# Kernel tuning notes

Measured on AMD Instinct MI355X. Metric: run time of the kernel, lower is better.

Reference implementation:

```python
import jax, jax.numpy as jnp
import numpy as np

KEEP_RATIO = 0.7  # fully-annealed keep ratio (epoch >= 2*warmup_epochs)


def setup_inputs() -> dict:
    key = jax.random.key(0)
    k0, k1, k2 = jax.random.split(key, 3)
    B, H, W, C, HID = 16, 128, 128, 256, 128
    N = H * W
    tokens = jax.random.normal(k0, (B, N, C), dtype=jnp.float32)
    # xavier_uniform-ish init for the scorer MLP
    lim1 = float(np.sqrt(6.0 / (C + HID)))
    lim2 = float(np.sqrt(6.0 / (HID + 1)))
    w1 = jax.random.uniform(k1, (C, HID), minval=-lim1, maxval=lim1, dtype=jnp.float32)
    b1 = jnp.zeros((HID,), dtype=jnp.float32)
    w2 = jax.random.uniform(k2, (HID, 1), minval=-lim2, maxval=lim2, dtype=jnp.float32)
    b2 = jnp.zeros((1,), dtype=jnp.float32)
    return {"tokens": tokens, "w1": w1, "b1": b1, "w2": w2, "b2": b2}


def reference(tokens, w1, b1, w2, b2):
    # tokens: [B, N, C]; importance scorer: fc1 -> GELU(exact) -> fc2 -> squeeze
    B, N, C = tokens.shape
    num_keep = int(N * KEEP_RATIO)  # static; min_tokens=10 << num_keep
    h = jax.nn.gelu(jnp.einsum("bnc,ch->bnh", tokens, w1) + b1, approximate=False)
    scores = (jnp.einsum("bnh,ho->bno", h, w2) + b2)[..., 0]  # [B, N]
    # top-k token selection, then sort kept indices to preserve spatial order
    _, top_idx = jax.lax.top_k(scores, num_keep)          # [B, K]
    kept_indices = jnp.sort(top_idx, axis=-1)              # [B, K]
    pruned_tokens = jnp.take_along_axis(tokens, kept_indices[..., None], axis=1)  # [B, K, C]
    return pruned_tokens, kept_indices, scores
```

## Files before the change

kernel.cpp:

```cpp
#include <hip/hip_runtime.h>
#include <math.h>

#define B_ 16
#define N_ 16384
#define C_ 256
#define H_ 128
#define K_ 11468
#define G_ ((B_ * N_) / 16)
#define GPB_ 16
#define NBLK_ (G_ / GPB_)

typedef __attribute__((ext_vector_type(8))) short s16x8;
typedef __attribute__((ext_vector_type(4))) float f32x4;
typedef __attribute__((ext_vector_type(4))) unsigned int u32x4;

__device__ __forceinline__ unsigned short f2bf(float f) {
  unsigned u = __builtin_bit_cast(unsigned, f);
  return (unsigned short)((u + 0x7FFFu + ((u >> 16) & 1u)) >> 16);
}
__device__ __forceinline__ unsigned fkey(float f) {
  unsigned u = __builtin_bit_cast(unsigned, f);
  return (u & 0x80000000u) ? ~u : (u | 0x80000000u);
}
__device__ __forceinline__ unsigned pk2(float hi, float lo) {
  return __builtin_amdgcn_perm(__builtin_bit_cast(unsigned, hi),
                               __builtin_bit_cast(unsigned, lo), 0x07060302u);
}

#define LDS_BARRIER()                                     \
  do {                                                    \
    asm volatile("s_waitcnt lgkmcnt(0)" ::: "memory");    \
    __builtin_amdgcn_s_barrier();                         \
  } while (0)

__device__ __forceinline__ float gelu_fast(float h) {
  const float t = 0.5f * h * h;
  const float u = 0.147f * t;
  const float num = t * (1.2732395f + u);
  const float den = 1.0f + u;
  const float r = num * __builtin_amdgcn_rcpf(den);
  const float e = __builtin_amdgcn_exp2f(r * -1.44269504f);
  const float s = __builtin_amdgcn_sqrtf(fmaxf(1.0f - e, 0.0f));
  const unsigned sgn = __builtin_bit_cast(unsigned, h) & 0x80000000u;
  const float erfv = __builtin_bit_cast(float, __builtin_bit_cast(unsigned, s) | sgn);
  return 0.5f * h * (1.0f + erfv);
}

__global__ void k_prep(const float* __restrict__ w1, unsigned short* __restrict__ w1t) {
  int i = blockIdx.x * blockDim.x + threadIdx.x;
  if (i < C_ * H_) {
    int c = i / H_, h = i % H_;
    w1t[h * C_ + c] = f2bf(w1[i]);
  }
}

__global__ __launch_bounds__(256) void k_score(
    const float* __restrict__ tokens, const unsigned short* __restrict__ w1t,
    const float* __restrict__ b1, const float* __restrict__ w2,
    const float* __restrict__ b2, float* __restrict__ scores_out) {
  __shared__ unsigned short lds_a[2][8 * 64 * 8];
  __shared__ float lds_c[4][16];

  const int tid = threadIdx.x;
  const int lane = tid & 63;
  const int l15 = lane & 15;
  const int l4 = lane >> 4;
  const int w = tid >> 6;

  s16x8 bfr0[8], bfr1[8];
  const int row0 = (2 * w) * 16 + l15;
  const int row1 = row0 + 16;
#pragma unroll
  for (int kk = 0; kk < 8; ++kk) {
    bfr0[kk] = *reinterpret_cast<const s16x8*>(w1t + row0 * 256 + (l4 + 4 * kk) * 8);
    bfr1[kk] = *reinterpret_cast<const s16x8*>(w1t + row1 * 256 + (l4 + 4 * kk) * 8);
  }
  const float b1v0 = b1[row0], b1v1 = b1[row1];
  const float w2v0 = w2[row0], w2v1 = w2[row1];
  const float b2v = b2[0];

  const int t = tid & 15;
  const int s = tid >> 4;
  const int g0 = blockIdx.x * GPB_;
  const float* tg = tokens + ((size_t)(g0 * 16 + t)) * 256 + s * 16;
  const int lb0 = (2 * s) * 128 + t * 8;
  const int lb1 = lb0 + 128;

  f32x4 vv[4];
  {
#pragma unroll
    for (int q = 0; q < 4; ++q) vv[q] = *reinterpret_cast<const f32x4*>(tg + 4 * q);
    u32x4 o0, o1;
    o0[0] = pk2(vv[0][1], vv[0][0]);
    o0[1] = pk2(vv[0][3], vv[0][2]);
    o0[2] = pk2(vv[1][1], vv[1][0]);
    o0[3] = pk2(vv[1][3], vv[1][2]);
    o1[0] = pk2(vv[2][1], vv[2][0]);
    o1[1] = pk2(vv[2][3], vv[2][2]);
    o1[2] = pk2(vv[3][1], vv[3][0]);
    o1[3] = pk2(vv[3][3], vv[3][2]);
    *reinterpret_cast<u32x4*>(&lds_a[0][lb0]) = o0;
    *reinterpret_cast<u32x4*>(&lds_a[0][lb1]) = o1;
  }
  LDS_BARRIER();

  int cur = 0;
  for (int i = 0; i < GPB_; ++i) {
    const int g = g0 + i;
    if (i + 1 < GPB_) {
      const float* p = tg + (size_t)(i + 1) * 4096;
#pragma unroll
      for (int q = 0; q < 4; ++q) vv[q] = *reinterpret_cast<const f32x4*>(p + 4 * q);
    }

    f32x4 acc0 = (f32x4){0.f, 0.f, 0.f, 0.f};
    f32x4 acc1 = (f32x4){0.f, 0.f, 0.f, 0.f};
#pragma unroll
    for (int kk = 0; kk < 8; ++kk) {
      s16x8 a = *reinterpret_cast<const s16x8*>(&lds_a[cur][(kk * 64 + lane) * 8]);
      acc0 = __builtin_amdgcn_mfma_f32_16x16x32_bf16(a, bfr0[kk], acc0, 0, 0, 0);
      acc1 = __builtin_amdgcn_mfma_f32_16x16x32_bf16(a, bfr1[kk], acc1, 0, 0, 0);
    }

    float p4[4];
#pragma unroll
    for (int rr = 0; rr < 4; ++rr) {
      float sp = gelu_fast(acc0[rr] + b1v0) * w2v0 + gelu_fast(acc1[rr] + b1v1) * w2v1;
      sp += __shfl_xor(sp, 1);
      sp += __shfl_xor(sp, 2);
      sp += __shfl_xor(sp, 4);
      sp += __shfl_xor(sp, 8);
      p4[rr] = sp;
    }
    if (l15 == 0) {
#pragma unroll
      for (int rr = 0; rr < 4; ++rr) lds_c[w][l4 * 4 + rr] = p4[rr];
    }
    LDS_BARRIER();

    if (tid < 16) {
      scores_out[g * 16 + tid] =
          lds_c[0][tid] + lds_c[1][tid] + lds_c[2][tid] + lds_c[3][tid] + b2v;
    }
    if (i + 1 < GPB_) {
      u32x4 o0, o1;
      o0[0] = pk2(vv[0][1], vv[0][0]);
      o0[1] = pk2(vv[0][3], vv[0][2]);
      o0[2] = pk2(vv[1][1], vv[1][0]);
      o0[3] = pk2(vv[1][3], vv[1][2]);
      o1[0] = pk2(vv[2][1], vv[2][0]);
      o1[1] = pk2(vv[2][3], vv[2][2]);
      o1[2] = pk2(vv[3][1], vv[3][0]);
      o1[3] = pk2(vv[3][3], vv[3][2]);
      *reinterpret_cast<u32x4*>(&lds_a[cur ^ 1][lb0]) = o0;
      *reinterpret_cast<u32x4*>(&lds_a[cur ^ 1][lb1]) = o1;
    }
    LDS_BARRIER();
    cur ^= 1;
  }
}

__device__ unsigned block_exscan_1024(unsigned v, volatile unsigned* wsum) {
  const int tid = threadIdx.x;
  const int lane = tid & 63;
  const int w = tid >> 6;
  unsigned x = v;
#pragma unroll
  for (int d = 1; d < 64; d <<= 1) {
    unsigned t = __shfl_up(x, d);
    if (lane >= d) x += t;
  }
  if (lane == 63) wsum[w] = x;
  __syncthreads();
  if (tid < 16) {
    unsigned s = wsum[tid];
#pragma unroll
    for (int d = 1; d < 16; d <<= 1) {
      unsigned u = __shfl_up(s, d);
      if (tid >= d) s += u;
    }
    wsum[tid] = s;
  }
  __syncthreads();
  unsigned r = (w ? wsum[w - 1] : 0u) + x - v;
  __syncthreads();
  return r;
}

__global__ __launch_bounds__(1024) void k_select(const float* __restrict__ scores_f,
                                                 int* __restrict__ kept,
                                                 float* __restrict__ out_idx) {
  __shared__ unsigned hist[2048];
  __shared__ unsigned wsum[16];
  __shared__ unsigned sh_T, sh_need;
  const int b = blockIdx.x;
  const int tid = threadIdx.x;
  const float* sp = scores_f + (size_t)b * N_;

  hist[tid] = 0; hist[tid + 1024] = 0;
  __syncthreads();
  for (int i = tid; i < N_; i += 1024) atomicAdd(&hist[fkey(sp[i]) >> 21], 1u);
  __syncthreads();
  {
    const int hi = 2047 - 2 * tid, lo = hi - 1;
    const unsigned chi = hist[hi], pair = chi + hist[lo];
    unsigned before = block_exscan_1024(pair, wsum);
    if (before < K_ && before + chi >= K_) { sh_T = (unsigned)hi; sh_need = K_ - before; }
    else if (before + chi < K_ && before + pair >= K_) { sh_T = (unsigned)lo; sh_need = K_ - before - chi; }
  }
  __syncthreads();
  const unsigned T0 = sh_T;
  unsigned needK = sh_need;
  __syncthreads();

  hist[tid] = 0; hist[tid + 1024] = 0;
  __syncthreads();
  for (int i = tid; i < N_; i += 1024) {
    unsigned k = fkey(sp[i]);
    if ((k >> 21) == T0) atomicAdd(&hist[(k >> 10) & 2047u], 1u);
  }
  __syncthreads();
  {
    const int hi = 2047 - 2 * tid, lo = hi - 1;
    const unsigned chi = hist[hi], pair = chi + hist[lo];
    unsigned before = block_exscan_1024(pair, wsum);
    if (before < needK && before + chi >= needK) { sh_T = (unsigned)hi; sh_need = needK - before; }
    else if (before + chi < needK && before + pair >= needK) { sh_T = (unsigned)lo; sh_need = needK - before - chi; }
  }
  __syncthreads();
  const unsigned P21 = (T0 << 11) | sh_T;
  needK = sh_need;
  __syncthreads();

  hist[tid] = 0;
  __syncthreads();
  for (int i = tid; i < N_; i += 1024) {
    unsigned k = fkey(sp[i]);
    if ((k >> 10) == P21) atomicAdd(&hist[k & 1023u], 1u);
  }
  __syncthreads();
  {
    const int hi = 1023 - tid;
    const unsigned chi = hist[hi];
    unsigned before = block_exscan_1024(chi, wsum);
    if (before < needK && before + chi >= needK) { sh_T = (unsigned)hi; sh_need = needK - before; }
  }
  __syncthreads();
  const unsigned Tkey = (P21 << 10) | sh_T;
  const unsigned need = sh_need;
  __syncthreads();

  const int i0 = tid * 16;
  unsigned cgt = 0, ceq = 0;
  for (int j = 0; j < 16; ++j) {
    unsigned k = fkey(sp[i0 + j]);
    cgt += (k > Tkey);
    ceq += (k == Tkey);
  }
  unsigned packed = block_exscan_1024((cgt << 16) | ceq, wsum);
  unsigned gt_b = packed >> 16;
  unsigned eq_b = packed & 0xFFFFu;
  for (int j = 0; j < 16; ++j) {
    unsigned k = fkey(sp[i0 + j]);
    if (k > Tkey) {
      unsigned pos = gt_b + (eq_b < need ? eq_b : need);
      kept[(size_t)b * K_ + pos] = i0 + j;
      out_idx[(size_t)b * K_ + pos] = (float)(i0 + j);
      ++gt_b;
    } else if (k == Tkey) {
      if (eq_b < need) {
        unsigned pos = gt_b + eq_b;
        kept[(size_t)b * K_ + pos] = i0 + j;
        out_idx[(size_t)b * K_ + pos] = (float)(i0 + j);
      }
      ++eq_b;
    }
  }
}

__global__ __launch_bounds__(256) void k_gather(const float* __restrict__ tokens,
                                                const int* __restrict__ kept,
                                                float* __restrict__ outp) {
  const int wid = (blockIdx.x * blockDim.x + threadIdx.x) >> 6;
  const int lane = threadIdx.x & 63;
  if (wid >= B_ * K_) return;
  const int b = wid / K_;
  const int idx = kept[wid];
  const f32x4 v = *reinterpret_cast<const f32x4*>(tokens + ((size_t)b * N_ + idx) * C_ + lane * 4);
  *reinterpret_cast<f32x4*>(outp + (size_t)wid * C_ + lane * 4) = v;
}

extern "C" void kernel_launch(void* const* d_in, const int* in_sizes, int n_in,
                              void* d_out, int out_size, void* d_ws, size_t ws_size,
                              hipStream_t stream) {
  const float* tokens = (const float*)d_in[0];
  const float* w1 = (const float*)d_in[1];
  const float* b1 = (const float*)d_in[2];
  const float* w2 = (const float*)d_in[3];
  const float* b2 = (const float*)d_in[4];

  float* out = (float*)d_out;
  float* out_pruned = out;
  float* out_idx = out + (size_t)B_ * K_ * C_;
  float* out_scores = out_idx + (size_t)B_ * K_;

  char* ws = (char*)d_ws;
  unsigned short* w1t = (unsigned short*)ws;
  int* kept = (int*)(ws + 0x10000);

  k_prep<<<dim3((C_ * H_ + 255) / 256), dim3(256), 0, stream>>>(w1, w1t);
  k_score<<<dim3(NBLK_), dim3(256), 0, stream>>>(tokens, w1t, b1, w2, b2, out_scores);
  k_select<<<dim3(B_), dim3(1024), 0, stream>>>(out_scores, kept, out_idx);
  k_gather<<<dim3((B_ * K_ + 3) / 4), dim3(256), 0, stream>>>(tokens, kept, out_pruned);
}
```

Measured before the change: 159.2 us.

## Replace three-pass radix select with one histogram pass plus candidate ranking

```diff
diff --git a/kernel.cpp b/kernel.cpp
--- a/kernel.cpp
+++ b/kernel.cpp
@@ -192,7 +192,7 @@
                                                  float* __restrict__ out_idx) {
   __shared__ unsigned hist[2048];
   __shared__ unsigned wsum[16];
-  __shared__ unsigned sh_T, sh_need;
+  __shared__ unsigned sh_T, sh_need, sh_m;
   const int b = blockIdx.x;
   const int tid = threadIdx.x;
   const float* sp = scores_f + (size_t)b * N_;
@@ -207,73 +207,70 @@
     unsigned before = block_exscan_1024(pair, wsum);
     if (before < K_ && before + chi >= K_) { sh_T = (unsigned)hi; sh_need = K_ - before; }
     else if (before + chi < K_ && before + pair >= K_) { sh_T = (unsigned)lo; sh_need = K_ - before - chi; }
+    if (tid == 0) sh_m = 0;
   }
   __syncthreads();
   const unsigned T0 = sh_T;
-  unsigned needK = sh_need;
-  __syncthreads();
-
-  hist[tid] = 0; hist[tid + 1024] = 0;
-  __syncthreads();
-  for (int i = tid; i < N_; i += 1024) {
-    unsigned k = fkey(sp[i]);
-    if ((k >> 21) == T0) atomicAdd(&hist[(k >> 10) & 2047u], 1u);
-  }
-  __syncthreads();
-  {
-    const int hi = 2047 - 2 * tid, lo = hi - 1;
-    const unsigned chi = hist[hi], pair = chi + hist[lo];
-    unsigned before = block_exscan_1024(pair, wsum);
-    if (before < needK && before + chi >= needK) { sh_T = (unsigned)hi; sh_need = needK - before; }
-    else if (before + chi < needK && before + pair >= needK) { sh_T = (unsigned)lo; sh_need = needK - before - chi; }
-  }
-  __syncthreads();
-  const unsigned P21 = (T0 << 11) | sh_T;
-  needK = sh_need;
-  __syncthreads();
-
-  hist[tid] = 0;
-  __syncthreads();
-  for (int i = tid; i < N_; i += 1024) {
-    unsigned k = fkey(sp[i]);
-    if ((k >> 10) == P21) atomicAdd(&hist[k & 1023u], 1u);
-  }
-  __syncthreads();
-  {
-    const int hi = 1023 - tid;
-    const unsigned chi = hist[hi];
-    unsigned before = block_exscan_1024(chi, wsum);
-    if (before < needK && before + chi >= needK) { sh_T = (unsigned)hi; sh_need = needK - before; }
-  }
-  __syncthreads();
-  const unsigned Tkey = (P21 << 10) | sh_T;
   const unsigned need = sh_need;
   __syncthreads();
 
+  unsigned* cand = hist;
   const int i0 = tid * 16;
-  unsigned cgt = 0, ceq = 0;
+  unsigned cgt = 0;
   for (int j = 0; j < 16; ++j) {
     unsigned k = fkey(sp[i0 + j]);
-    cgt += (k > Tkey);
-    ceq += (k == Tkey);
-  }
-  unsigned packed = block_exscan_1024((cgt << 16) | ceq, wsum);
-  unsigned gt_b = packed >> 16;
-  unsigned eq_b = packed & 0xFFFFu;
+    unsigned bin = k >> 21;
+    cgt += (bin > T0);
+    if (bin == T0) {
+      unsigned e = atomicAdd(&sh_m, 1u);
+      if (e < 1024u) { cand[2 * e] = k; cand[2 * e + 1] = (unsigned)(i0 + j); }
+    }
+  }
+  unsigned gt_base = block_exscan_1024(cgt, wsum);
+  const unsigned m = (sh_m < 1024u) ? sh_m : 1024u;
+
+  for (unsigned e = tid; e < m; e += 1024) {
+    const unsigned ke = cand[2 * e];
+    const unsigned ie = cand[2 * e + 1] & 0x7FFFFFFFu;
+    unsigned r = 0;
+    for (unsigned f = 0; f < m; ++f) {
+      const unsigned kf = cand[2 * f];
+      const unsigned fi = cand[2 * f + 1] & 0x7FFFFFFFu;
+      r += (kf > ke) || (kf == ke && fi < ie);
+    }
+    if (r < need) cand[2 * e + 1] |= 0x80000000u;
+  }
+  __syncthreads();
+
+  unsigned gt_run = gt_base;
   for (int j = 0; j < 16; ++j) {
-    unsigned k = fkey(sp[i0 + j]);
-    if (k > Tkey) {
-      unsigned pos = gt_b + (eq_b < need ? eq_b : need);
-      kept[(size_t)b * K_ + pos] = i0 + j;
-      out_idx[(size_t)b * K_ + pos] = (float)(i0 + j);
-      ++gt_b;
-    } else if (k == Tkey) {
-      if (eq_b < need) {
-        unsigned pos = gt_b + eq_b;
-        kept[(size_t)b * K_ + pos] = i0 + j;
-        out_idx[(size_t)b * K_ + pos] = (float)(i0 + j);
+    const unsigned i = (unsigned)(i0 + j);
+    const unsigned k = fkey(sp[i0 + j]);
+    const unsigned bin = k >> 21;
+    if (bin > T0) {
+      unsigned eqb = 0;
+      for (unsigned f = 0; f < m; ++f) {
+        const unsigned fi = cand[2 * f + 1];
+        eqb += (fi >> 31) & ((fi & 0x7FFFFFFFu) < i);
       }
-      ++eq_b;
+      const unsigned pos = gt_run + eqb;
+      kept[(size_t)b * K_ + pos] = (int)i;
+      out_idx[(size_t)b * K_ + pos] = (float)i;
+      ++gt_run;
+    } else if (bin == T0) {
+      unsigned eqb = 0, sel = 0;
+      for (unsigned f = 0; f < m; ++f) {
+        const unsigned fi = cand[2 * f + 1];
+        const unsigned fidx = fi & 0x7FFFFFFFu;
+        const unsigned flg = fi >> 31;
+        eqb += flg & (fidx < i);
+        sel |= flg & (fidx == i);
+      }
+      if (sel) {
+        const unsigned pos = gt_run + eqb;
+        kept[(size_t)b * K_ + pos] = (int)i;
+        out_idx[(size_t)b * K_ + pos] = (float)i;
+      }
     }
   }
 }
```

New measurement: 238.7 us. 1.5x slower.

## Stream token tiles into LDS with async global_load_lds and convert at MFMA time

Applied to the files above, without the earlier changes.

```diff
diff --git a/kernel.cpp b/kernel.cpp
--- a/kernel.cpp
+++ b/kernel.cpp
@@ -32,6 +32,12 @@
     asm volatile("s_waitcnt lgkmcnt(0)" ::: "memory");    \
     __builtin_amdgcn_s_barrier();                         \
   } while (0)
+
+__device__ __forceinline__ void async_copy16(const float* g, float* l) {
+  __builtin_amdgcn_global_load_lds(
+      (const __attribute__((address_space(1))) unsigned int*)g,
+      (__attribute__((address_space(3))) unsigned int*)l, 16, 0, 0);
+}
 
 __device__ __forceinline__ float gelu_fast(float h) {
   const float t = 0.5f * h * h;
@@ -58,7 +64,7 @@
     const float* __restrict__ tokens, const unsigned short* __restrict__ w1t,
     const float* __restrict__ b1, const float* __restrict__ w2,
     const float* __restrict__ b2, float* __restrict__ scores_out) {
-  __shared__ unsigned short lds_a[2][8 * 64 * 8];
+  __shared__ float lds_f[2][4096];
   __shared__ float lds_c[4][16];
 
   const int tid = threadIdx.x;
@@ -79,45 +85,51 @@
   const float w2v0 = w2[row0], w2v1 = w2[row1];
   const float b2v = b2[0];
 
-  const int t = tid & 15;
-  const int s = tid >> 4;
   const int g0 = blockIdx.x * GPB_;
-  const float* tg = tokens + ((size_t)(g0 * 16 + t)) * 256 + s * 16;
-  const int lb0 = (2 * s) * 128 + t * 8;
-  const int lb1 = lb0 + 128;
-
-  f32x4 vv[4];
-  {
-#pragma unroll
-    for (int q = 0; q < 4; ++q) vv[q] = *reinterpret_cast<const f32x4*>(tg + 4 * q);
-    u32x4 o0, o1;
-    o0[0] = pk2(vv[0][1], vv[0][0]);
-    o0[1] = pk2(vv[0][3], vv[0][2]);
-    o0[2] = pk2(vv[1][1], vv[1][0]);
-    o0[3] = pk2(vv[1][3], vv[1][2]);
-    o1[0] = pk2(vv[2][1], vv[2][0]);
-    o1[1] = pk2(vv[2][3], vv[2][2]);
-    o1[2] = pk2(vv[3][1], vv[3][0]);
-    o1[3] = pk2(vv[3][3], vv[3][2]);
-    *reinterpret_cast<u32x4*>(&lds_a[0][lb0]) = o0;
-    *reinterpret_cast<u32x4*>(&lds_a[0][lb1]) = o1;
-  }
-  LDS_BARRIER();
+  const float* gbase = tokens + (size_t)g0 * 16 * 256;
+
+  int st_[4], sc_[4];
+#pragma unroll
+  for (int r = 0; r < 4; ++r) {
+    const int sslot = (w * 4 + r) * 64 + lane;
+    st_[r] = sslot & 15;
+    sc_[r] = sslot >> 4;
+  }
+
+  const int sbase = 32 * l4 + l15;
+
+#pragma unroll
+  for (int r = 0; r < 4; ++r) {
+    async_copy16(gbase + st_[r] * 256 + sc_[r] * 4,
+                 &lds_f[0][(size_t)((w * 4 + r) * 64 + lane) * 4]);
+  }
+  __syncthreads();
 
   int cur = 0;
   for (int i = 0; i < GPB_; ++i) {
     const int g = g0 + i;
     if (i + 1 < GPB_) {
-      const float* p = tg + (size_t)(i + 1) * 4096;
-#pragma unroll
-      for (int q = 0; q < 4; ++q) vv[q] = *reinterpret_cast<const f32x4*>(p + 4 * q);
-    }
-
+      const float* gp = gbase + (size_t)(i + 1) * 4096;
+#pragma unroll
+      for (int r = 0; r < 4; ++r) {
+        async_copy16(gp + st_[r] * 256 + sc_[r] * 4,
+                     &lds_f[cur ^ 1][(size_t)((w * 4 + r) * 64 + lane) * 4]);
+      }
+    }
+
+    const f32x4* bufp = reinterpret_cast<const f32x4*>(&lds_f[cur][0]);
     f32x4 acc0 = (f32x4){0.f, 0.f, 0.f, 0.f};
     f32x4 acc1 = (f32x4){0.f, 0.f, 0.f, 0.f};
 #pragma unroll
     for (int kk = 0; kk < 8; ++kk) {
-      s16x8 a = *reinterpret_cast<const s16x8*>(&lds_a[cur][(kk * 64 + lane) * 8]);
+      const f32x4 va = bufp[sbase + 128 * kk];
+      const f32x4 vb = bufp[sbase + 128 * kk + 16];
+      u32x4 o;
+      o[0] = pk2(va[1], va[0]);
+      o[1] = pk2(va[3], va[2]);
+      o[2] = pk2(vb[1], vb[0]);
+      o[3] = pk2(vb[3], vb[2]);
+      const s16x8 a = __builtin_bit_cast(s16x8, o);
       acc0 = __builtin_amdgcn_mfma_f32_16x16x32_bf16(a, bfr0[kk], acc0, 0, 0, 0);
       acc1 = __builtin_amdgcn_mfma_f32_16x16x32_bf16(a, bfr1[kk], acc1, 0, 0, 0);
     }
@@ -142,20 +154,7 @@
       scores_out[g * 16 + tid] =
           lds_c[0][tid] + lds_c[1][tid] + lds_c[2][tid] + lds_c[3][tid] + b2v;
     }
-    if (i + 1 < GPB_) {
-      u32x4 o0, o1;
-      o0[0] = pk2(vv[0][1], vv[0][0]);
-      o0[1] = pk2(vv[0][3], vv[0][2]);
-      o0[2] = pk2(vv[1][1], vv[1][0]);
-      o0[3] = pk2(vv[1][3], vv[1][2]);
-      o1[0] = pk2(vv[2][1], vv[2][0]);
-      o1[1] = pk2(vv[2][3], vv[2][2]);
-      o1[2] = pk2(vv[3][1], vv[3][0]);
-      o1[3] = pk2(vv[3][3], vv[3][2]);
-      *reinterpret_cast<u32x4*>(&lds_a[cur ^ 1][lb0]) = o0;
-      *reinterpret_cast<u32x4*>(&lds_a[cur ^ 1][lb1]) = o1;
-    }
-    LDS_BARRIER();
+    __syncthreads();
     cur ^= 1;
   }
 }
```

Result: no change. 161.3 us (+1.3%).
